# Performance work log

Hardware: AMD Instinct MI355X
Metric: run time of the kernel (lower is better)

The kernel has to match this reference:

```python
import jax, jax.numpy as jnp
import numpy as np

DIM = 512
HEADS = 8
HEAD_DIM = DIM // HEADS
SCALE = HEAD_DIM ** -0.5
B, N = 256, 144


def setup_inputs() -> dict:
    key = jax.random.key(0)
    k1, k2, k3, k4, k5, k6 = jax.random.split(key, 6)
    x = jax.random.normal(k1, (B, N, DIM), dtype=jnp.float32)
    topo_all_fea = jax.random.normal(k2, (B, N, DIM), dtype=jnp.float32)
    # nn.Linear weights stored as [out, in]
    kv_w = jax.random.normal(k3, (2 * DIM, DIM), dtype=jnp.float32) * 0.02
    q_w = jax.random.normal(k4, (DIM, DIM), dtype=jnp.float32) * 0.02
    proj_w = jax.random.normal(k5, (DIM, DIM), dtype=jnp.float32) * 0.02
    proj_b = jax.random.normal(k6, (DIM,), dtype=jnp.float32) * 0.02
    return {"x": x, "topo_all_fea": topo_all_fea, "kv_w": kv_w,
            "q_w": q_w, "proj_w": proj_w, "proj_b": proj_b, "is_end": 1}


def reference(x, topo_all_fea, kv_w, q_w, proj_w, proj_b, is_end):
    # block_pos == 'end' -> add topology features to the KV stream
    x_topo = x + topo_all_fea if is_end else x
    b, n, d = x.shape
    # kv: [B,N,2D] -> [2,B,H,N,hd]
    kv = (x_topo @ kv_w.T).reshape(b, n, 2, HEADS, HEAD_DIM).transpose(2, 0, 3, 1, 4)
    k, v = kv[0], kv[1]
    # q: [B,N,D] -> [B,H,N,hd]
    q = (x @ q_w.T).reshape(b, n, HEADS, HEAD_DIM).transpose(0, 2, 1, 3)
    # manual attention in fp32 (autocast(False) region in the original)
    attn = jnp.einsum('bhqd,bhkd->bhqk', q, k) * SCALE
    attn = jax.nn.softmax(attn, axis=-1)
    out = jnp.einsum('bhqk,bhkd->bhqd', attn, v)  # [B,H,N,hd]
    out = out.transpose(0, 2, 1, 3).reshape(b, n, d)
    return out @ proj_w.T + proj_b
```

## Files before the change

kernel.cpp:

```cpp
#include <hip/hip_runtime.h>
#include <hip/hip_bf16.h>

typedef float  f32x4  __attribute__((ext_vector_type(4)));
typedef __bf16 bf16x8 __attribute__((ext_vector_type(8)));
typedef __bf16 bf16x4 __attribute__((ext_vector_type(4)));

#define D_  512
#define H_  8
#define HD_ 64
#define B_  256
#define N_  144
#define M_  (B_*N_)

using gptr_t = const __attribute__((address_space(1))) char*;
using lptr_t = __attribute__((address_space(3))) char*;
#define GLDS16(gp, lp) __builtin_amdgcn_global_load_lds((gptr_t)(gp), (lptr_t)(lp), 16, 0, 0)

__global__ void prep_weights_kernel(const float* __restrict__ kvw,
                                    const float* __restrict__ qw,
                                    const float* __restrict__ pw,
                                    __bf16* __restrict__ kvb,
                                    __bf16* __restrict__ qb,
                                    __bf16* __restrict__ pb) {
    int idx = blockIdx.x * 256 + threadIdx.x;
    const float* s; __bf16* d; int off;
    if (idx < 131072)      { s = kvw; d = kvb; off = idx; }
    else if (idx < 196608) { s = qw;  d = qb;  off = idx - 131072; }
    else                   { s = pw;  d = pb;  off = idx - 196608; }
    f32x4 v = *(const f32x4*)(s + (size_t)off * 4);
    bf16x4 o;
    o[0] = (__bf16)v.x; o[1] = (__bf16)v.y; o[2] = (__bf16)v.z; o[3] = (__bf16)v.w;
    *(bf16x4*)(d + (size_t)off * 4) = o;
}

__global__ void prep_act_kernel(const float* __restrict__ x,
                                const float* __restrict__ topo,
                                const int* __restrict__ is_end,
                                __bf16* __restrict__ xb,
                                __bf16* __restrict__ ab) {
    const float tf = (is_end[0] != 0) ? 1.f : 0.f;
    const size_t total = (size_t)M_ * D_ / 8;
    for (size_t i = (size_t)blockIdx.x * 256 + threadIdx.x; i < total;
         i += (size_t)gridDim.x * 256) {
        f32x4 a0 = *(const f32x4*)(x + i * 8);
        f32x4 a1 = *(const f32x4*)(x + i * 8 + 4);
        f32x4 t0 = *(const f32x4*)(topo + i * 8);
        f32x4 t1 = *(const f32x4*)(topo + i * 8 + 4);
        bf16x8 xo, ao;
#pragma unroll
        for (int j = 0; j < 4; ++j) {
            xo[j]     = (__bf16)a0[j];
            xo[j + 4] = (__bf16)a1[j];
            ao[j]     = (__bf16)(a0[j] + tf * t0[j]);
            ao[j + 4] = (__bf16)(a1[j] + tf * t1[j]);
        }
        *(bf16x8*)(xb + i * 8) = xo;
        *(bf16x8*)(ab + i * 8) = ao;
    }
}

template<int MODE>
__launch_bounds__(256, 3)
__global__ void mm_kernel(const __bf16* __restrict__ ab,
                          const __bf16* __restrict__ xb,
                          const __bf16* __restrict__ kvb,
                          const __bf16* __restrict__ qb,
                          __bf16* __restrict__ kout,
                          __bf16* __restrict__ vTout,
                          __bf16* __restrict__ qout,
                          const float* __restrict__ bias,
                          float* __restrict__ pout) {
    __shared__ __bf16 As[128 * 64];
    __shared__ __bf16 Bs[128 * 64];

    const int tid  = threadIdx.x;
    const int lane = tid & 63;
    const int wid  = tid >> 6;
    const int lrow = lane & 15, lhi = lane >> 4;
    const int wr   = wid >> 1,  wc  = wid & 1;

    const int NB  = (MODE == 0) ? 12 : 4;
    const int per = (MODE == 0) ? 432 : 144;
    const int bid = blockIdx.x;
    const int wg  = (bid & 7) * per + (bid >> 3);
    const int mb  = wg / NB;
    const int nb  = wg - mb * NB;
    const int m0  = mb * 128;

    const __bf16* Ap;
    const __bf16* Bp;
    if (MODE == 0) {
        Ap = (nb < 8) ? ab : xb;
        Bp = (nb < 8) ? (kvb + (size_t)nb * 128 * D_) : (qb + (size_t)(nb - 8) * 128 * D_);
    } else {
        Ap = ab;
        Bp = kvb + (size_t)nb * 128 * D_;
    }

    f32x4 acc[4][4];
#pragma unroll
    for (int i = 0; i < 4; ++i)
#pragma unroll
        for (int j = 0; j < 4; ++j) acc[i][j] = (f32x4){0.f, 0.f, 0.f, 0.f};

    const int srow = lane >> 3;
    const int scol = (lane & 7) * 16;

    for (int kt = 0; kt < 8; ++kt) {
        const int k0 = kt * 64;
        const char* Agb = (const char*)(Ap + (size_t)m0 * D_ + k0);
        const char* Bgb = (const char*)(Bp + k0);
#pragma unroll
        for (int j = 0; j < 4; ++j) {
            const int chunk = wid * 4 + j;
            const int row   = chunk * 8 + srow;
            GLDS16(Agb + (size_t)row * (D_ * 2) + scol, (char*)As + chunk * 1024);
            GLDS16(Bgb + (size_t)row * (D_ * 2) + scol, (char*)Bs + chunk * 1024);
        }
        __syncthreads();
#pragma unroll
        for (int kk = 0; kk < 2; ++kk) {
            bf16x8 af[4], bfr[4];
#pragma unroll
            for (int mi = 0; mi < 4; ++mi)
                af[mi] = *(const bf16x8*)((const char*)As +
                          (wr * 64 + mi * 16 + lrow) * 128 + kk * 64 + lhi * 16);
#pragma unroll
            for (int ni = 0; ni < 4; ++ni)
                bfr[ni] = *(const bf16x8*)((const char*)Bs +
                          (wc * 64 + ni * 16 + lrow) * 128 + kk * 64 + lhi * 16);
#pragma unroll
            for (int mi = 0; mi < 4; ++mi)
#pragma unroll
                for (int ni = 0; ni < 4; ++ni)
                    acc[mi][ni] = __builtin_amdgcn_mfma_f32_16x16x32_bf16(
                        af[mi], bfr[ni], acc[mi][ni], 0, 0, 0);
        }
        __syncthreads();
    }

    float bv4[4];
    if (MODE == 1) {
#pragma unroll
        for (int ni = 0; ni < 4; ++ni) bv4[ni] = bias[nb * 128 + wc * 64 + ni * 16 + lrow];
    }
#pragma unroll
    for (int mi = 0; mi < 4; ++mi) {
#pragma unroll
        for (int reg = 0; reg < 4; ++reg) {
            int m  = m0 + wr * 64 + mi * 16 + lhi * 4 + reg;
            int bb = m / N_;
            int nn = m - bb * N_;
#pragma unroll
            for (int ni = 0; ni < 4; ++ni) {
                const int ol = wc * 64 + ni * 16 + lrow;
                float val = acc[mi][ni][reg];
                if (MODE == 0) {
                    const int o = nb * 128 + ol;
                    if (nb < 8) {
                        int hh = (o >> 6) & 7;
                        int dd = o & 63;
                        if (o < 512)
                            kout[(((size_t)bb * H_ + hh) * N_ + nn) * HD_ + dd] = (__bf16)val;
                        else
                            vTout[(((size_t)bb * H_ + hh) * HD_ + dd) * N_ + nn] = (__bf16)val;
                    } else {
                        int o2 = o - 1024;
                        int hh = o2 >> 6, dd = o2 & 63;
                        qout[(((size_t)bb * H_ + hh) * N_ + nn) * HD_ + dd] = (__bf16)val;
                    }
                } else {
                    pout[(size_t)m * D_ + nb * 128 + ol] = val + bv4[ni];
                }
            }
        }
    }
}

__launch_bounds__(256, 2)
__global__ void attn_kernel(const __bf16* __restrict__ qbuf,
                            const __bf16* __restrict__ kbuf,
                            const __bf16* __restrict__ vTbuf,
                            __bf16* __restrict__ aout) {
    __shared__ __bf16 Ks[144][72];
    __shared__ __bf16 Vs[64][168];
    __shared__ __bf16 Ps[4][16][160];

    const int tid  = threadIdx.x;
    const int lane = tid & 63, wid = tid >> 6;
    const int lrow = lane & 15, lhi = lane >> 4;
    const int bh = blockIdx.x;
    const int bb = bh >> 3, hh = bh & 7;

    const __bf16* kg = kbuf  + (size_t)bh * (N_ * HD_);
    const __bf16* vg = vTbuf + (size_t)bh * (N_ * HD_);
    const __bf16* qg = qbuf  + (size_t)bh * (N_ * HD_);

    for (int c = tid; c < 1152; c += 256) {
        int row = c >> 3, cc = c & 7;
        *(bf16x8*)&Ks[row][cc * 8] = *(const bf16x8*)(kg + row * 64 + cc * 8);
    }
    for (int c = tid; c < 1152; c += 256) {
        int dd = c / 18, cc = c - dd * 18;
        *(bf16x8*)&Vs[dd][cc * 8] = *(const bf16x8*)(vg + dd * 144 + cc * 8);
    }
    bf16x8 z8;
#pragma unroll
    for (int i = 0; i < 8; ++i) z8[i] = (__bf16)0.f;
    if (tid < 192) {
        int dd = tid / 3, cc = tid - dd * 3;
        *(bf16x8*)&Vs[dd][144 + cc * 8] = z8;
    }
    if (lhi < 2)
        *(bf16x8*)&Ps[wid][lrow][144 + lhi * 8] = z8;
    __syncthreads();

    const float sc = 0.125f * 1.44269504089f;

    for (int t = wid; t < 9; t += 4) {
        bf16x8 aq[2];
#pragma unroll
        for (int kk = 0; kk < 2; ++kk)
            aq[kk] = *(const bf16x8*)(qg + (t * 16 + lrow) * 64 + kk * 32 + lhi * 8);

        f32x4 s[9];
#pragma unroll
        for (int j = 0; j < 9; ++j) s[j] = (f32x4){0.f, 0.f, 0.f, 0.f};
#pragma unroll
        for (int j = 0; j < 9; ++j)
#pragma unroll
            for (int kk = 0; kk < 2; ++kk)
                s[j] = __builtin_amdgcn_mfma_f32_16x16x32_bf16(
                    aq[kk], *(const bf16x8*)&Ks[j * 16 + lrow][kk * 32 + lhi * 8], s[j], 0, 0, 0);

        float inv[4];
#pragma unroll
        for (int reg = 0; reg < 4; ++reg) {
            float mx = s[0][reg];
#pragma unroll
            for (int j = 1; j < 9; ++j) mx = fmaxf(mx, s[j][reg]);
#pragma unroll
            for (int off = 1; off < 16; off <<= 1) mx = fmaxf(mx, __shfl_xor(mx, off, 16));
            float sum = 0.f;
#pragma unroll
            for (int j = 0; j < 9; ++j) {
                float p = exp2f((s[j][reg] - mx) * sc);
                s[j][reg] = p;
                sum += p;
            }
#pragma unroll
            for (int off = 1; off < 16; off <<= 1) sum += __shfl_xor(sum, off, 16);
            inv[reg] = 1.f / sum;
        }
#pragma unroll
        for (int j = 0; j < 9; ++j)
#pragma unroll
            for (int reg = 0; reg < 4; ++reg)
                Ps[wid][lhi * 4 + reg][j * 16 + lrow] = (__bf16)(s[j][reg] * inv[reg]);

#pragma unroll
        for (int dc = 0; dc < 4; ++dc) {
            f32x4 o4 = (f32x4){0.f, 0.f, 0.f, 0.f};
#pragma unroll
            for (int kc = 0; kc < 5; ++kc)
                o4 = __builtin_amdgcn_mfma_f32_16x16x32_bf16(
                    *(const bf16x8*)&Ps[wid][lrow][kc * 32 + lhi * 8],
                    *(const bf16x8*)&Vs[dc * 16 + lrow][kc * 32 + lhi * 8], o4, 0, 0, 0);
#pragma unroll
            for (int reg = 0; reg < 4; ++reg) {
                int nn = t * 16 + lhi * 4 + reg;
                int dd = dc * 16 + lrow;
                aout[((size_t)bb * N_ + nn) * D_ + hh * HD_ + dd] = (__bf16)o4[reg];
            }
        }
    }
}

extern "C" void kernel_launch(void* const* d_in, const int* in_sizes, int n_in,
                              void* d_out, int out_size, void* d_ws, size_t ws_size,
                              hipStream_t stream) {
    const float* x      = (const float*)d_in[0];
    const float* topo   = (const float*)d_in[1];
    const float* kvw    = (const float*)d_in[2];
    const float* qw     = (const float*)d_in[3];
    const float* pw     = (const float*)d_in[4];
    const float* pb     = (const float*)d_in[5];
    const int*   is_end = (const int*)d_in[6];
    float* out = (float*)d_out;

    char* ws = (char*)d_ws;
    __bf16* kvb = (__bf16*)(ws);
    __bf16* qb  = (__bf16*)(ws + (1u << 20));
    __bf16* pwb = (__bf16*)(ws + (1u << 20) + 524288);
    size_t off = (1u << 20) + 2 * 524288;
    const size_t BUF = (size_t)M_ * D_ * 2;
    __bf16* xb    = (__bf16*)(ws + off); off += BUF;
    __bf16* ab    = (__bf16*)(ws + off); off += BUF;
    __bf16* kbuf  = (__bf16*)(ws + off); off += BUF;
    __bf16* vTbuf = (__bf16*)(ws + off); off += BUF;
    __bf16* qbuf  = (__bf16*)(ws + off); off += BUF;
    __bf16* abuf  = xb;

    prep_weights_kernel<<<1024, 256, 0, stream>>>(kvw, qw, pw, kvb, qb, pwb);
    prep_act_kernel<<<2048, 256, 0, stream>>>(x, topo, is_end, xb, ab);
    mm_kernel<0><<<3456, 256, 0, stream>>>(ab, xb, kvb, qb,
                                           kbuf, vTbuf, qbuf, nullptr, nullptr);
    attn_kernel<<<2048, 256, 0, stream>>>(qbuf, kbuf, vTbuf, abuf);
    mm_kernel<1><<<1152, 256, 0, stream>>>(abuf, nullptr, pwb, nullptr,
                                           nullptr, nullptr, nullptr, pb, out);
}
```

Measured before the change: 399.9 us.

## Double-buffer GEMM LDS tiles and split attention into one-wave blocks per query tile

The GEMM kernels now keep two LDS buffers per operand and issue the next k-tile's global-to-LDS loads before computing on the current one, which drops one barrier per iteration. The goal is to overlap memory latency with MFMA work, at the cost of twice the LDS and an occupancy hint lowered from 3 to 2. The attention kernel is split into 18432 single-wave blocks, one per (batch, head, query tile), with an XCD-aware index remap. K and V are now read straight from global memory instead of being staged through LDS. This removes the staging and block-wide sync but re-reads K and V nine times per head, relying on cache.

```diff
diff --git a/kernel.cpp b/kernel.cpp
--- a/kernel.cpp
+++ b/kernel.cpp
@@ -60,18 +60,17 @@
 }
 
 template<int MODE>
-__launch_bounds__(256, 3)
-__global__ void mm_kernel(const __bf16* __restrict__ ab,
-                          const __bf16* __restrict__ xb,
-                          const __bf16* __restrict__ kvb,
-                          const __bf16* __restrict__ qb,
-                          __bf16* __restrict__ kout,
-                          __bf16* __restrict__ vTout,
-                          __bf16* __restrict__ qout,
-                          const float* __restrict__ bias,
-                          float* __restrict__ pout) {
-    __shared__ __bf16 As[128 * 64];
-    __shared__ __bf16 Bs[128 * 64];
+__device__ __forceinline__ void mm_body(const __bf16* __restrict__ ab,
+                                        const __bf16* __restrict__ xb,
+                                        const __bf16* __restrict__ kvb,
+                                        const __bf16* __restrict__ qb,
+                                        __bf16* __restrict__ kout,
+                                        __bf16* __restrict__ vTout,
+                                        __bf16* __restrict__ qout,
+                                        const float* __restrict__ bias,
+                                        float* __restrict__ pout) {
+    __shared__ __bf16 As[2][128 * 64];
+    __shared__ __bf16 Bs[2][128 * 64];
 
     const int tid  = threadIdx.x;
     const int lane = tid & 63;
@@ -106,7 +105,7 @@
     const int srow = lane >> 3;
     const int scol = (lane & 7) * 16;
 
-    for (int kt = 0; kt < 8; ++kt) {
+    auto stage = [&](int buf, int kt) {
         const int k0 = kt * 64;
         const char* Agb = (const char*)(Ap + (size_t)m0 * D_ + k0);
         const char* Bgb = (const char*)(Bp + k0);
@@ -114,20 +113,26 @@
         for (int j = 0; j < 4; ++j) {
             const int chunk = wid * 4 + j;
             const int row   = chunk * 8 + srow;
-            GLDS16(Agb + (size_t)row * (D_ * 2) + scol, (char*)As + chunk * 1024);
-            GLDS16(Bgb + (size_t)row * (D_ * 2) + scol, (char*)Bs + chunk * 1024);
-        }
+            GLDS16(Agb + (size_t)row * (D_ * 2) + scol, (char*)As[buf] + chunk * 1024);
+            GLDS16(Bgb + (size_t)row * (D_ * 2) + scol, (char*)Bs[buf] + chunk * 1024);
+        }
+    };
+
+    stage(0, 0);
+    int cur = 0;
+    for (int kt = 0; kt < 8; ++kt) {
         __syncthreads();
+        if (kt < 7) stage(cur ^ 1, kt + 1);
 #pragma unroll
         for (int kk = 0; kk < 2; ++kk) {
             bf16x8 af[4], bfr[4];
 #pragma unroll
             for (int mi = 0; mi < 4; ++mi)
-                af[mi] = *(const bf16x8*)((const char*)As +
+                af[mi] = *(const bf16x8*)((const char*)As[cur] +
                           (wr * 64 + mi * 16 + lrow) * 128 + kk * 64 + lhi * 16);
 #pragma unroll
             for (int ni = 0; ni < 4; ++ni)
-                bfr[ni] = *(const bf16x8*)((const char*)Bs +
+                bfr[ni] = *(const bf16x8*)((const char*)Bs[cur] +
                           (wc * 64 + ni * 16 + lrow) * 128 + kk * 64 + lhi * 16);
 #pragma unroll
             for (int mi = 0; mi < 4; ++mi)
@@ -136,7 +141,7 @@
                     acc[mi][ni] = __builtin_amdgcn_mfma_f32_16x16x32_bf16(
                         af[mi], bfr[ni], acc[mi][ni], 0, 0, 0);
         }
-        __syncthreads();
+        cur ^= 1;
     }
 
     float bv4[4];
@@ -177,101 +182,104 @@
     }
 }
 
-__launch_bounds__(256, 2)
+__global__ __launch_bounds__(256, 2) void mm0_kernel(
+        const __bf16* __restrict__ ab, const __bf16* __restrict__ xb,
+        const __bf16* __restrict__ kvb, const __bf16* __restrict__ qb,
+        __bf16* __restrict__ kout, __bf16* __restrict__ vTout,
+        __bf16* __restrict__ qout) {
+    mm_body<0>(ab, xb, kvb, qb, kout, vTout, qout, nullptr, nullptr);
+}
+
+__global__ __launch_bounds__(256, 2) void mm1_kernel(
+        const __bf16* __restrict__ ab, const __bf16* __restrict__ pwb,
+        const float* __restrict__ bias, float* __restrict__ pout) {
+    mm_body<1>(ab, nullptr, pwb, nullptr, nullptr, nullptr, nullptr, bias, pout);
+}
+
+__launch_bounds__(64)
 __global__ void attn_kernel(const __bf16* __restrict__ qbuf,
                             const __bf16* __restrict__ kbuf,
                             const __bf16* __restrict__ vTbuf,
                             __bf16* __restrict__ aout) {
-    __shared__ __bf16 Ks[144][72];
-    __shared__ __bf16 Vs[64][168];
-    __shared__ __bf16 Ps[4][16][160];
-
-    const int tid  = threadIdx.x;
-    const int lane = tid & 63, wid = tid >> 6;
+    __shared__ __bf16 Ps[16][168];
+
+    const int lane = threadIdx.x & 63;
     const int lrow = lane & 15, lhi = lane >> 4;
-    const int bh = blockIdx.x;
-    const int bb = bh >> 3, hh = bh & 7;
+    const int bid  = blockIdx.x;
+    const int w    = (bid & 7) * 2304 + (bid >> 3);
+    const int bh   = w / 9;
+    const int t    = w - bh * 9;
+    const int bb   = bh >> 3, hh = bh & 7;
 
     const __bf16* kg = kbuf  + (size_t)bh * (N_ * HD_);
     const __bf16* vg = vTbuf + (size_t)bh * (N_ * HD_);
     const __bf16* qg = qbuf  + (size_t)bh * (N_ * HD_);
 
-    for (int c = tid; c < 1152; c += 256) {
-        int row = c >> 3, cc = c & 7;
-        *(bf16x8*)&Ks[row][cc * 8] = *(const bf16x8*)(kg + row * 64 + cc * 8);
-    }
-    for (int c = tid; c < 1152; c += 256) {
-        int dd = c / 18, cc = c - dd * 18;
-        *(bf16x8*)&Vs[dd][cc * 8] = *(const bf16x8*)(vg + dd * 144 + cc * 8);
-    }
     bf16x8 z8;
 #pragma unroll
     for (int i = 0; i < 8; ++i) z8[i] = (__bf16)0.f;
-    if (tid < 192) {
-        int dd = tid / 3, cc = tid - dd * 3;
-        *(bf16x8*)&Vs[dd][144 + cc * 8] = z8;
-    }
-    if (lhi < 2)
-        *(bf16x8*)&Ps[wid][lrow][144 + lhi * 8] = z8;
-    __syncthreads();
+    if (lane < 32)
+        *(bf16x8*)&Ps[lane >> 1][144 + (lane & 1) * 8] = z8;
 
     const float sc = 0.125f * 1.44269504089f;
 
-    for (int t = wid; t < 9; t += 4) {
-        bf16x8 aq[2];
+    bf16x8 aq[2];
+#pragma unroll
+    for (int kk = 0; kk < 2; ++kk)
+        aq[kk] = *(const bf16x8*)(qg + (t * 16 + lrow) * 64 + kk * 32 + lhi * 8);
+
+    f32x4 s[9];
+#pragma unroll
+    for (int j = 0; j < 9; ++j) s[j] = (f32x4){0.f, 0.f, 0.f, 0.f};
+#pragma unroll
+    for (int j = 0; j < 9; ++j)
 #pragma unroll
         for (int kk = 0; kk < 2; ++kk)
-            aq[kk] = *(const bf16x8*)(qg + (t * 16 + lrow) * 64 + kk * 32 + lhi * 8);
-
-        f32x4 s[9];
-#pragma unroll
-        for (int j = 0; j < 9; ++j) s[j] = (f32x4){0.f, 0.f, 0.f, 0.f};
-#pragma unroll
-        for (int j = 0; j < 9; ++j)
-#pragma unroll
-            for (int kk = 0; kk < 2; ++kk)
-                s[j] = __builtin_amdgcn_mfma_f32_16x16x32_bf16(
-                    aq[kk], *(const bf16x8*)&Ks[j * 16 + lrow][kk * 32 + lhi * 8], s[j], 0, 0, 0);
-
-        float inv[4];
+            s[j] = __builtin_amdgcn_mfma_f32_16x16x32_bf16(
+                aq[kk],
+                *(const bf16x8*)(kg + (j * 16 + lrow) * 64 + kk * 32 + lhi * 8),
+                s[j], 0, 0, 0);
+
+    float inv[4];
+#pragma unroll
+    for (int reg = 0; reg < 4; ++reg) {
+        float mx = s[0][reg];
+#pragma unroll
+        for (int j = 1; j < 9; ++j) mx = fmaxf(mx, s[j][reg]);
+#pragma unroll
+        for (int off = 1; off < 16; off <<= 1) mx = fmaxf(mx, __shfl_xor(mx, off, 16));
+        float sum = 0.f;
+#pragma unroll
+        for (int j = 0; j < 9; ++j) {
+            float p = exp2f((s[j][reg] - mx) * sc);
+            s[j][reg] = p;
+            sum += p;
+        }
+#pragma unroll
+        for (int off = 1; off < 16; off <<= 1) sum += __shfl_xor(sum, off, 16);
+        inv[reg] = 1.f / sum;
+    }
+
+#pragma unroll
+    for (int j = 0; j < 9; ++j)
+#pragma unroll
+        for (int reg = 0; reg < 4; ++reg)
+            Ps[lhi * 4 + reg][j * 16 + lrow] = (__bf16)(s[j][reg] * inv[reg]);
+
+#pragma unroll
+    for (int dc = 0; dc < 4; ++dc) {
+        f32x4 o4 = (f32x4){0.f, 0.f, 0.f, 0.f};
+#pragma unroll
+        for (int kc = 0; kc < 5; ++kc)
+            o4 = __builtin_amdgcn_mfma_f32_16x16x32_bf16(
+                *(const bf16x8*)&Ps[lrow][kc * 32 + lhi * 8],
+                *(const bf16x8*)(vg + (dc * 16 + lrow) * 144 + kc * 32 + lhi * 8),
+                o4, 0, 0, 0);
 #pragma unroll
         for (int reg = 0; reg < 4; ++reg) {
-            float mx = s[0][reg];
-#pragma unroll
-            for (int j = 1; j < 9; ++j) mx = fmaxf(mx, s[j][reg]);
-#pragma unroll
-            for (int off = 1; off < 16; off <<= 1) mx = fmaxf(mx, __shfl_xor(mx, off, 16));
-            float sum = 0.f;
-#pragma unroll
-            for (int j = 0; j < 9; ++j) {
-                float p = exp2f((s[j][reg] - mx) * sc);
-                s[j][reg] = p;
-                sum += p;
-            }
-#pragma unroll
-            for (int off = 1; off < 16; off <<= 1) sum += __shfl_xor(sum, off, 16);
-            inv[reg] = 1.f / sum;
-        }
-#pragma unroll
-        for (int j = 0; j < 9; ++j)
-#pragma unroll
-            for (int reg = 0; reg < 4; ++reg)
-                Ps[wid][lhi * 4 + reg][j * 16 + lrow] = (__bf16)(s[j][reg] * inv[reg]);
-
-#pragma unroll
-        for (int dc = 0; dc < 4; ++dc) {
-            f32x4 o4 = (f32x4){0.f, 0.f, 0.f, 0.f};
-#pragma unroll
-            for (int kc = 0; kc < 5; ++kc)
-                o4 = __builtin_amdgcn_mfma_f32_16x16x32_bf16(
-                    *(const bf16x8*)&Ps[wid][lrow][kc * 32 + lhi * 8],
-                    *(const bf16x8*)&Vs[dc * 16 + lrow][kc * 32 + lhi * 8], o4, 0, 0, 0);
-#pragma unroll
-            for (int reg = 0; reg < 4; ++reg) {
-                int nn = t * 16 + lhi * 4 + reg;
-                int dd = dc * 16 + lrow;
-                aout[((size_t)bb * N_ + nn) * D_ + hh * HD_ + dd] = (__bf16)o4[reg];
-            }
+            int nn = t * 16 + lhi * 4 + reg;
+            int dd = dc * 16 + lrow;
+            aout[((size_t)bb * N_ + nn) * D_ + hh * HD_ + dd] = (__bf16)o4[reg];
         }
     }
 }
@@ -303,9 +311,7 @@
 
     prep_weights_kernel<<<1024, 256, 0, stream>>>(kvw, qw, pw, kvb, qb, pwb);
     prep_act_kernel<<<2048, 256, 0, stream>>>(x, topo, is_end, xb, ab);
-    mm_kernel<0><<<3456, 256, 0, stream>>>(ab, xb, kvb, qb,
-                                           kbuf, vTbuf, qbuf, nullptr, nullptr);
-    attn_kernel<<<2048, 256, 0, stream>>>(qbuf, kbuf, vTbuf, abuf);
-    mm_kernel<1><<<1152, 256, 0, stream>>>(abuf, nullptr, pwb, nullptr,
-                                           nullptr, nullptr, nullptr, pb, out);
-}
+    mm0_kernel<<<3456, 256, 0, stream>>>(ab, xb, kvb, qb, kbuf, vTbuf, qbuf);
+    attn_kernel<<<18432, 64, 0, stream>>>(qbuf, kbuf, vTbuf, abuf);
+    mm1_kernel<<<1152, 256, 0, stream>>>(abuf, pwb, pb, out);
+}
```

Result: slower. 442.2 us (+10.6%).
